# Kernel optimization log

Measured on AMD Instinct MI355X. Metric: run time of the kernel, lower is better.

The kernel has to match this reference:

```python
import jax, jax.numpy as jnp
import numpy as np

N_NODES, N_EDGES, D, N_RELS = 50000, 600000, 128, 460


def setup_inputs() -> dict:
    key = jax.random.key(0)
    ks = jax.random.split(key, 8)
    h = jax.random.normal(ks[0], (N_NODES, D), dtype=jnp.float32)
    emb_rel = jax.random.normal(ks[1], (N_RELS, D), dtype=jnp.float32)
    attn_fc_w = jax.random.normal(ks[2], (D, 3 * D), dtype=jnp.float32) * 0.05   # Linear(3D->D), weight [out,in]
    attn_fc2_w = jax.random.normal(ks[3], (1, D), dtype=jnp.float32) * 0.05     # Linear(D->1)
    loop_weight = jax.random.normal(ks[4], (D, D), dtype=jnp.float32) * 0.05
    edge_src = jax.random.randint(ks[5], (N_EDGES,), 0, N_NODES)
    edge_dst = jax.random.randint(ks[6], (N_EDGES,), 0, N_NODES)
    edge_type = jax.random.randint(ks[7], (N_EDGES,), 0, N_RELS)
    return {"h": h, "emb_rel": emb_rel, "attn_fc_w": attn_fc_w,
            "attn_fc2_w": attn_fc2_w, "loop_weight": loop_weight,
            "edge_src": edge_src, "edge_dst": edge_dst, "edge_type": edge_type}


def reference(h, emb_rel, attn_fc_w, attn_fc2_w, loop_weight, edge_src, edge_dst, edge_type):
    n = h.shape[0]
    # --- per-edge gather ---
    hs = h[edge_src]            # [E, D] src features (mailbox 'e_h')
    ht = h[edge_dst]            # [E, D]
    rel = emb_rel[edge_type]    # [E, D]
    # --- concat-MLP attention: leaky_relu(fc2(fc1([hs|ht|rel]))) ---
    z2 = jnp.concatenate([hs, ht, rel], axis=1)          # [E, 3D]
    a = z2 @ attn_fc_w.T                                  # [E, D]
    e = jax.nn.leaky_relu(a @ attn_fc2_w.T)               # [E, 1], slope 0.01 (torch default)
    # --- per-destination segment softmax ---
    m = jax.ops.segment_max(e, edge_dst, num_segments=n)  # [N, 1]
    m = jnp.where(jnp.isfinite(m), m, jnp.float32(0.0))   # empty nodes -> -inf; neutralize
    ex = jnp.exp(e - m[edge_dst])                         # [E, 1]
    den = jax.ops.segment_sum(ex, edge_dst, num_segments=n)
    alpha = ex / den[edge_dst]                            # [E, 1]
    # --- weighted scatter-sum of src features ---
    node_repr = jax.ops.segment_sum(alpha * hs, edge_dst, num_segments=n)  # [N, D]
    # --- self-loop ---
    node_repr = node_repr + h @ loop_weight
    return node_repr
```

## Files before the change

kernel.cpp:

```cpp
#include <hip/hip_runtime.h>

#define N_NODES 50000
#define N_EDGES 600000
#define D 128
#define N_RELS 460
#define CAP_LOG 6

typedef unsigned short u16;
typedef __attribute__((ext_vector_type(8))) short bf16x8;
typedef __attribute__((ext_vector_type(4))) float f32x4;

enum : int {
    OFF_W      = 0,
    OFF_S1     = 384,
    OFF_S2     = 50384,
    OFF_S3     = 100384,
    OFF_COUNTS = 100864,
    OFF_RANK   = 150864,
    OFF_CSR    = 750864,
    OFF_HB     = 3950864,
    OFF_WT     = 7150864,
};

#define NODE_WAVES   12500
#define REL_WAVES    115
#define SCORE_BLOCKS 3154
#define CNT_BLOCKS   586
#define ZERO_BLOCKS  196
#define FILL_BLOCKS  1172
#define GEMM_BLOCKS  782

__device__ __forceinline__ u16 f2bf(float f) {
    unsigned u = __float_as_uint(f);
    unsigned r = u + 0x7FFFu + ((u >> 16) & 1u);
    return (u16)(r >> 16);
}

__global__ void k_prep(const float* __restrict__ fc1, const float* __restrict__ fc2,
                       const float* __restrict__ W,
                       float* __restrict__ w, u16* __restrict__ wt,
                       int* __restrict__ counts) {
    int b = blockIdx.x, t = threadIdx.x;
    if (b == 0) {
        for (int j = t; j < 3 * D; j += 256) {
            float acc = 0.f;
            for (int k = 0; k < D; ++k) acc += fc2[k] * fc1[k * 3 * D + j];
            w[j] = acc;
        }
    } else if (b <= 64) {
        int i = (b - 1) * 256 + t;
        int k = i >> 7, n = i & 127;
        wt[n * D + k] = f2bf(W[k * D + n]);
    } else {
        int i = (b - 65) * 256 + t;
        if (i < N_NODES) counts[i] = 0;
    }
}

__global__ void k_count(const int* __restrict__ dst, int* __restrict__ counts,
                        int* __restrict__ rank) {
    int i = blockIdx.x * blockDim.x + threadIdx.x;
    if (i < N_EDGES / 4) {
        int4 d4 = ((const int4*)dst)[i];
        int4 r4;
        r4.x = atomicAdd(&counts[d4.x], 1);
        r4.y = atomicAdd(&counts[d4.y], 1);
        r4.z = atomicAdd(&counts[d4.z], 1);
        r4.w = atomicAdd(&counts[d4.w], 1);
        ((int4*)rank)[i] = r4;
    }
}

__global__ __launch_bounds__(256) void k_fused(
        const int* __restrict__ src, const int* __restrict__ dst,
        const int* __restrict__ typ, const int* __restrict__ rank,
        unsigned* __restrict__ csr,
        const float* __restrict__ h, const float* __restrict__ emb_rel,
        const float* __restrict__ w,
        float* __restrict__ s1, float* __restrict__ s2, float* __restrict__ s3,
        u16* __restrict__ hb, const u16* __restrict__ wt,
        float* __restrict__ out) {
    if (blockIdx.x < FILL_BLOCKS) {
        int i = blockIdx.x * blockDim.x + threadIdx.x;
        if (i >= N_EDGES / 2) return;
        int2 d2  = ((const int2*)dst)[i];
        int2 s2v = ((const int2*)src)[i];
        int2 t2  = ((const int2*)typ)[i];
        int2 r2  = ((const int2*)rank)[i];
        csr[(d2.x << CAP_LOG) + r2.x] = (unsigned)s2v.x | ((unsigned)t2.x << 16);
        csr[(d2.y << CAP_LOG) + r2.y] = (unsigned)s2v.y | ((unsigned)t2.y << 16);
    } else if (blockIdx.x < FILL_BLOCKS + GEMM_BLOCKS) {
        int b = blockIdx.x - FILL_BLOCKS;
        int t = threadIdx.x;
        int wave = t >> 6, lane = t & 63;
        int quad = lane >> 4, m16 = lane & 15;
        int nbase = b * 64 + wave * 16;

        f32x4 acc[8];
        #pragma unroll
        for (int cg = 0; cg < 8; ++cg) acc[cg] = (f32x4){0.f, 0.f, 0.f, 0.f};

        int arow = nbase + m16;
        if (arow >= N_NODES) arow = N_NODES - 1;
        const float* aptr = h + (size_t)arow * D + quad * 8;

        #pragma unroll
        for (int k0 = 0; k0 < D; k0 += 32) {
            float4 a0 = *(const float4*)(aptr + k0);
            float4 a1 = *(const float4*)(aptr + k0 + 4);
            bf16x8 a;
            a[0] = (short)f2bf(a0.x); a[1] = (short)f2bf(a0.y);
            a[2] = (short)f2bf(a0.z); a[3] = (short)f2bf(a0.w);
            a[4] = (short)f2bf(a1.x); a[5] = (short)f2bf(a1.y);
            a[6] = (short)f2bf(a1.z); a[7] = (short)f2bf(a1.w);
            #pragma unroll
            for (int cg = 0; cg < 8; ++cg) {
                bf16x8 bb = *(const bf16x8*)(&wt[(size_t)(cg * 16 + m16) * D + k0 + quad * 8]);
                acc[cg] = __builtin_amdgcn_mfma_f32_16x16x32_bf16(a, bb, acc[cg], 0, 0, 0);
            }
        }
        #pragma unroll
        for (int reg = 0; reg < 4; ++reg) {
            int row = nbase + quad * 4 + reg;
            if (row < N_NODES) {
                #pragma unroll
                for (int cg = 0; cg < 8; ++cg)
                    out[(size_t)row * D + cg * 16 + m16] = acc[cg][reg];
            }
        }
    } else {
        int wv = ((blockIdx.x - FILL_BLOCKS - GEMM_BLOCKS) * blockDim.x + threadIdx.x) >> 6;
        int l  = threadIdx.x & 63;
        int sub = l >> 4;
        int q   = l & 15;
        if (wv < NODE_WAVES) {
            int r = wv * 4 + sub;
            const float* hp = h + (size_t)r * D + q * 8;
            float4 h0 = *(const float4*)hp;
            float4 h1 = *(const float4*)(hp + 4);
            uint4 pk;
            pk.x = (unsigned)f2bf(h0.x) | ((unsigned)f2bf(h0.y) << 16);
            pk.y = (unsigned)f2bf(h0.z) | ((unsigned)f2bf(h0.w) << 16);
            pk.z = (unsigned)f2bf(h1.x) | ((unsigned)f2bf(h1.y) << 16);
            pk.w = (unsigned)f2bf(h1.z) | ((unsigned)f2bf(h1.w) << 16);
            ((uint4*)hb)[(size_t)r * 16 + q] = pk;
            float4 w10 = *(const float4*)(w + q * 8);
            float4 w11 = *(const float4*)(w + q * 8 + 4);
            float4 w20 = *(const float4*)(w + D + q * 8);
            float4 w21 = *(const float4*)(w + D + q * 8 + 4);
            float a1 = h0.x * w10.x + h0.y * w10.y + h0.z * w10.z + h0.w * w10.w
                     + h1.x * w11.x + h1.y * w11.y + h1.z * w11.z + h1.w * w11.w;
            float a2 = h0.x * w20.x + h0.y * w20.y + h0.z * w20.z + h0.w * w20.w
                     + h1.x * w21.x + h1.y * w21.y + h1.z * w21.z + h1.w * w21.w;
            #pragma unroll
            for (int o = 8; o; o >>= 1) { a1 += __shfl_xor(a1, o, 16); a2 += __shfl_xor(a2, o, 16); }
            if (q == 0) { s1[r] = a1; s2[r] = a2; }
        } else if (wv < NODE_WAVES + REL_WAVES) {
            int r = (wv - NODE_WAVES) * 4 + sub;
            const float* rp = emb_rel + (size_t)r * D + q * 8;
            float4 r0 = *(const float4*)rp;
            float4 r1 = *(const float4*)(rp + 4);
            float4 w30 = *(const float4*)(w + 2 * D + q * 8);
            float4 w31 = *(const float4*)(w + 2 * D + q * 8 + 4);
            float a3 = r0.x * w30.x + r0.y * w30.y + r0.z * w30.z + r0.w * w30.w
                     + r1.x * w31.x + r1.y * w31.y + r1.z * w31.z + r1.w * w31.w;
            #pragma unroll
            for (int o = 8; o; o >>= 1) a3 += __shfl_xor(a3, o, 16);
            if (q == 0) s3[r] = a3;
        }
    }
}

__global__ void k_gather(const u16* __restrict__ hb, const int* __restrict__ counts,
                         const unsigned* __restrict__ csr,
                         const float* __restrict__ s1, const float* __restrict__ s2,
                         const float* __restrict__ s3, float* __restrict__ out) {
    int n  = (blockIdx.x * blockDim.x + threadIdx.x) >> 4;
    int gl = threadIdx.x & 15;
    if (n >= N_NODES) return;
    int deg = counts[n];
    if (deg == 0) return;
    int beg = n << CAP_LOG;
    int end = beg + deg;

    float s2n = s2[n];
    float den = 0.f;
    f32x4 accA = {0.f, 0.f, 0.f, 0.f}, accB = {0.f, 0.f, 0.f, 0.f};

    for (int cb = beg; cb < end; cb += 16) {
        int i = cb + gl;
        int msrc = 0; float mex = 0.f;
        if (i < end) {
            unsigned p = csr[i];
            msrc = (int)(p & 0xFFFFu);
            float x = s1[msrc] + s2n + s3[p >> 16];
            float lv = (x > 0.f) ? x : 0.01f * x;
            mex = __expf(lv);
        }
        den += mex;
        int cnt = min(16, end - cb);
        int j = 0;
        for (; j + 3 < cnt; j += 4) {
            int   a0 = __shfl(msrc, j, 16),     a1 = __shfl(msrc, j + 1, 16);
            int   a2 = __shfl(msrc, j + 2, 16), a3 = __shfl(msrc, j + 3, 16);
            float c0 = __shfl(mex, j, 16),      c1 = __shfl(mex, j + 1, 16);
            float c2 = __shfl(mex, j + 2, 16),  c3 = __shfl(mex, j + 3, 16);
            uint4 u0 = ((const uint4*)(hb + (size_t)a0 * D))[gl];
            uint4 u1 = ((const uint4*)(hb + (size_t)a1 * D))[gl];
            uint4 u2 = ((const uint4*)(hb + (size_t)a2 * D))[gl];
            uint4 u3 = ((const uint4*)(hb + (size_t)a3 * D))[gl];
            accA.x += c0 * __uint_as_float(u0.x << 16) + c1 * __uint_as_float(u1.x << 16)
                    + c2 * __uint_as_float(u2.x << 16) + c3 * __uint_as_float(u3.x << 16);
            accA.y += c0 * __uint_as_float(u0.x & 0xFFFF0000u) + c1 * __uint_as_float(u1.x & 0xFFFF0000u)
                    + c2 * __uint_as_float(u2.x & 0xFFFF0000u) + c3 * __uint_as_float(u3.x & 0xFFFF0000u);
            accA.z += c0 * __uint_as_float(u0.y << 16) + c1 * __uint_as_float(u1.y << 16)
                    + c2 * __uint_as_float(u2.y << 16) + c3 * __uint_as_float(u3.y << 16);
            accA.w += c0 * __uint_as_float(u0.y & 0xFFFF0000u) + c1 * __uint_as_float(u1.y & 0xFFFF0000u)
                    + c2 * __uint_as_float(u2.y & 0xFFFF0000u) + c3 * __uint_as_float(u3.y & 0xFFFF0000u);
            accB.x += c0 * __uint_as_float(u0.z << 16) + c1 * __uint_as_float(u1.z << 16)
                    + c2 * __uint_as_float(u2.z << 16) + c3 * __uint_as_float(u3.z << 16);
            accB.y += c0 * __uint_as_float(u0.z & 0xFFFF0000u) + c1 * __uint_as_float(u1.z & 0xFFFF0000u)
                    + c2 * __uint_as_float(u2.z & 0xFFFF0000u) + c3 * __uint_as_float(u3.z & 0xFFFF0000u);
            accB.z += c0 * __uint_as_float(u0.w << 16) + c1 * __uint_as_float(u1.w << 16)
                    + c2 * __uint_as_float(u2.w << 16) + c3 * __uint_as_float(u3.w << 16);
            accB.w += c0 * __uint_as_float(u0.w & 0xFFFF0000u) + c1 * __uint_as_float(u1.w & 0xFFFF0000u)
                    + c2 * __uint_as_float(u2.w & 0xFFFF0000u) + c3 * __uint_as_float(u3.w & 0xFFFF0000u);
        }
        for (; j < cnt; ++j) {
            int   a0 = __shfl(msrc, j, 16);
            float c0 = __shfl(mex, j, 16);
            uint4 u0 = ((const uint4*)(hb + (size_t)a0 * D))[gl];
            accA.x += c0 * __uint_as_float(u0.x << 16);
            accA.y += c0 * __uint_as_float(u0.x & 0xFFFF0000u);
            accA.z += c0 * __uint_as_float(u0.y << 16);
            accA.w += c0 * __uint_as_float(u0.y & 0xFFFF0000u);
            accB.x += c0 * __uint_as_float(u0.z << 16);
            accB.y += c0 * __uint_as_float(u0.z & 0xFFFF0000u);
            accB.z += c0 * __uint_as_float(u0.w << 16);
            accB.w += c0 * __uint_as_float(u0.w & 0xFFFF0000u);
        }
    }
    #pragma unroll
    for (int o = 8; o; o >>= 1) den += __shfl_xor(den, o, 16);
    float inv = 1.f / den;

    float* op = out + (size_t)n * D + gl * 8;
    float4 o0 = *(float4*)op, o1 = *(float4*)(op + 4);
    o0.x += accA.x * inv; o0.y += accA.y * inv; o0.z += accA.z * inv; o0.w += accA.w * inv;
    o1.x += accB.x * inv; o1.y += accB.y * inv; o1.z += accB.z * inv; o1.w += accB.w * inv;
    *(float4*)op = o0; *(float4*)(op + 4) = o1;
}

extern "C" void kernel_launch(void* const* d_in, const int* in_sizes, int n_in,
                              void* d_out, int out_size, void* d_ws, size_t ws_size,
                              hipStream_t stream) {
    const float* h       = (const float*)d_in[0];
    const float* emb_rel = (const float*)d_in[1];
    const float* fc1     = (const float*)d_in[2];
    const float* fc2     = (const float*)d_in[3];
    const float* loopw   = (const float*)d_in[4];
    const int*   esrc    = (const int*)d_in[5];
    const int*   edst    = (const int*)d_in[6];
    const int*   etyp    = (const int*)d_in[7];
    float* out = (float*)d_out;
    float* ws  = (float*)d_ws;

    float*    w       = ws + OFF_W;
    float*    s1      = ws + OFF_S1;
    float*    s2      = ws + OFF_S2;
    float*    s3      = ws + OFF_S3;
    int*      counts  = (int*)(ws + OFF_COUNTS);
    int*      rank    = (int*)(ws + OFF_RANK);
    unsigned* csr     = (unsigned*)(ws + OFF_CSR);
    u16*      hb      = (u16*)(ws + OFF_HB);
    u16*      wt      = (u16*)(ws + OFF_WT);

    k_prep<<<1 + 64 + ZERO_BLOCKS, 256, 0, stream>>>(fc1, fc2, loopw, w, wt, counts);

    k_count<<<CNT_BLOCKS, 256, 0, stream>>>(edst, counts, rank);

    k_fused<<<FILL_BLOCKS + GEMM_BLOCKS + SCORE_BLOCKS, 256, 0, stream>>>(
        esrc, edst, etyp, rank, csr, h, emb_rel, w, s1, s2, s3, hb, wt, out);

    k_gather<<<(N_NODES * 16 + 255) / 256, 256, 0, stream>>>(
        hb, counts, csr, s1, s2, s3, out);
}
```

Before: 192.1 us.

## Merge edge counting into CSR fill with padded per-node atomic counters

Removes the separate counting kernel and its rank array. The fill blocks now claim CSR slots with atomicAdd directly on per-node counters. Each counter is padded to 16 ints (64 bytes) to reduce contention between neighbouring counters. This saves one kernel launch and the rank write/read pass, but the padding enlarges the counter array that must be zeroed (800k ints instead of 50k) and scatters the counter accesses across more cache lines. Slot order within each node becomes nondeterministic, which changes the order of floating-point summation.

```diff
diff --git a/kernel.cpp b/kernel.cpp
--- a/kernel.cpp
+++ b/kernel.cpp
@@ -16,17 +16,15 @@
     OFF_S2     = 50384,
     OFF_S3     = 100384,
     OFF_COUNTS = 100864,
-    OFF_RANK   = 150864,
-    OFF_CSR    = 750864,
-    OFF_HB     = 3950864,
-    OFF_WT     = 7150864,
+    OFF_CSR    = 900864,
+    OFF_HB     = 4100864,
+    OFF_WT     = 7300864,
 };
 
 #define NODE_WAVES   12500
 #define REL_WAVES    115
 #define SCORE_BLOCKS 3154
-#define CNT_BLOCKS   586
-#define ZERO_BLOCKS  196
+#define ZERO_BLOCKS  3125
 #define FILL_BLOCKS  1172
 #define GEMM_BLOCKS  782
 
@@ -53,27 +51,13 @@
         wt[n * D + k] = f2bf(W[k * D + n]);
     } else {
         int i = (b - 65) * 256 + t;
-        if (i < N_NODES) counts[i] = 0;
-    }
-}
-
-__global__ void k_count(const int* __restrict__ dst, int* __restrict__ counts,
-                        int* __restrict__ rank) {
-    int i = blockIdx.x * blockDim.x + threadIdx.x;
-    if (i < N_EDGES / 4) {
-        int4 d4 = ((const int4*)dst)[i];
-        int4 r4;
-        r4.x = atomicAdd(&counts[d4.x], 1);
-        r4.y = atomicAdd(&counts[d4.y], 1);
-        r4.z = atomicAdd(&counts[d4.z], 1);
-        r4.w = atomicAdd(&counts[d4.w], 1);
-        ((int4*)rank)[i] = r4;
+        if (i < N_NODES * 16) counts[i] = 0;
     }
 }
 
 __global__ __launch_bounds__(256) void k_fused(
         const int* __restrict__ src, const int* __restrict__ dst,
-        const int* __restrict__ typ, const int* __restrict__ rank,
+        const int* __restrict__ typ, int* __restrict__ counts,
         unsigned* __restrict__ csr,
         const float* __restrict__ h, const float* __restrict__ emb_rel,
         const float* __restrict__ w,
@@ -86,9 +70,10 @@
         int2 d2  = ((const int2*)dst)[i];
         int2 s2v = ((const int2*)src)[i];
         int2 t2  = ((const int2*)typ)[i];
-        int2 r2  = ((const int2*)rank)[i];
-        csr[(d2.x << CAP_LOG) + r2.x] = (unsigned)s2v.x | ((unsigned)t2.x << 16);
-        csr[(d2.y << CAP_LOG) + r2.y] = (unsigned)s2v.y | ((unsigned)t2.y << 16);
+        int slot0 = atomicAdd(&counts[d2.x << 4], 1);
+        int slot1 = atomicAdd(&counts[d2.y << 4], 1);
+        csr[(d2.x << CAP_LOG) + slot0] = (unsigned)s2v.x | ((unsigned)t2.x << 16);
+        csr[(d2.y << CAP_LOG) + slot1] = (unsigned)s2v.y | ((unsigned)t2.y << 16);
     } else if (blockIdx.x < FILL_BLOCKS + GEMM_BLOCKS) {
         int b = blockIdx.x - FILL_BLOCKS;
         int t = threadIdx.x;
@@ -178,7 +163,7 @@
     int n  = (blockIdx.x * blockDim.x + threadIdx.x) >> 4;
     int gl = threadIdx.x & 15;
     if (n >= N_NODES) return;
-    int deg = counts[n];
+    int deg = counts[n << 4];
     if (deg == 0) return;
     int beg = n << CAP_LOG;
     int end = beg + deg;
@@ -270,17 +255,14 @@
     float*    s2      = ws + OFF_S2;
     float*    s3      = ws + OFF_S3;
     int*      counts  = (int*)(ws + OFF_COUNTS);
-    int*      rank    = (int*)(ws + OFF_RANK);
     unsigned* csr     = (unsigned*)(ws + OFF_CSR);
     u16*      hb      = (u16*)(ws + OFF_HB);
     u16*      wt      = (u16*)(ws + OFF_WT);
 
     k_prep<<<1 + 64 + ZERO_BLOCKS, 256, 0, stream>>>(fc1, fc2, loopw, w, wt, counts);
 
-    k_count<<<CNT_BLOCKS, 256, 0, stream>>>(edst, counts, rank);
-
     k_fused<<<FILL_BLOCKS + GEMM_BLOCKS + SCORE_BLOCKS, 256, 0, stream>>>(
-        esrc, edst, etyp, rank, csr, h, emb_rel, w, s1, s2, s3, hb, wt, out);
+        esrc, edst, etyp, counts, csr, h, emb_rel, w, s1, s2, s3, hb, wt, out);
 
     k_gather<<<(N_NODES * 16 + 255) / 256, 256, 0, stream>>>(
         hb, counts, csr, s1, s2, s3, out);
```

Result: faster. 173.8 us (-9.5%).
